# Performance work log

Hardware: AMD Instinct MI355X
Metric: run time of the kernel (lower is better)

Reference implementation:

```python
import jax, jax.numpy as jnp
import numpy as np

N = 100000  # num_nodes


def setup_inputs() -> dict:
    key = jax.random.key(0)
    k1, k2, k3, k4 = jax.random.split(key, 4)
    nodes = jax.random.randint(k1, (10000,), 0, N)
    edge_index = jax.random.randint(k2, (2, 1600000), 0, N)
    emb_weight = jax.random.normal(k3, (N, 512), dtype=jnp.float32)
    W = jax.random.normal(k4, (512, 128), dtype=jnp.float32) * 0.05
    return {"nodes": nodes, "edge_index": edge_index, "emb_weight": emb_weight, "W": W}


def reference(nodes, edge_index, emb_weight, W):
    # GCNConv (PyG semantics, bias=False): add self-loops, symmetric deg
    # normalization, linear transform, scatter-add aggregation into targets.
    num_nodes = emb_weight.shape[0]
    loops = jnp.arange(num_nodes, dtype=edge_index.dtype)
    row = jnp.concatenate([edge_index[0], loops])  # sources (x_j)
    col = jnp.concatenate([edge_index[1], loops])  # targets (aggregation)

    ones = jnp.ones(row.shape[0], dtype=emb_weight.dtype)
    deg = jax.ops.segment_sum(ones, col, num_segments=num_nodes)
    dinv = jnp.where(deg > 0, jax.lax.rsqrt(deg), 0.0)
    norm = dinv[row] * dinv[col]  # [E+N]

    h = emb_weight @ W  # [N, C] dense transform (main GEMM)
    msg = h[row] * norm[:, None]  # gather + scale, [E+N, C]
    out = jax.ops.segment_sum(msg, col, num_segments=num_nodes)  # scatter-add
    return out[nodes]
```

## Files before the change

kernel.cpp:

```cpp
#include <hip/hip_runtime.h>
#include <hip/hip_bf16.h>


constexpr int KDIM = 512;
constexpr int CDIM = 128;
constexpr int CAPB = 64;
constexpr int CAPO = 16;

typedef __attribute__((ext_vector_type(8))) short short8;
typedef __attribute__((ext_vector_type(4))) float f32x4;

static __device__ __forceinline__ unsigned short f2bf(float f) {
    __hip_bfloat16 b = __float2bfloat16(f);
    return *reinterpret_cast<unsigned short*>(&b);
}
static __device__ __forceinline__ float bf2f(unsigned short b) {
    return __uint_as_float(((unsigned)b) << 16);
}

__global__ void k_init(int* __restrict__ deg, int* __restrict__ tmap,
                       int* __restrict__ cur, int* __restrict__ ocnt,
                       int* __restrict__ ucount,
                       const float* __restrict__ W, unsigned short* __restrict__ wt,
                       int N, int n) {
    int i = blockIdx.x * blockDim.x + threadIdx.x;
    if (i < N) { deg[i] = 0; tmap[i] = -1; }
    if (i < n) { cur[i] = 0; ocnt[i] = 0; }
    if (i == 0) *ucount = 0;
    if (i < 65536) {
        int j  = i & 7;
        int l  = (i >> 3) & 63;
        int st = i >> 9;
        int t  = st & 7, s = st >> 3;
        int k  = s * 32 + (l >> 4) * 8 + j;
        int c  = t * 16 + (l & 15);
        wt[i] = f2bf(W[(size_t)k * CDIM + c]);
    }
}

__global__ void k_targets(const int* __restrict__ nodes, int n,
                          int* __restrict__ tmap, int* __restrict__ tlist,
                          int* __restrict__ ucount) {
    int i = blockIdx.x * blockDim.x + threadIdx.x;
    if (i >= n) return;
    int v = nodes[i];
    if (atomicCAS(&tmap[v], -1, -2) == -1) {
        int slot = atomicAdd(ucount, 1);
        tlist[slot] = v;
        tmap[v] = slot;
    }
}

__global__ __launch_bounds__(256, 4)
void k_main(const float* __restrict__ emb, const unsigned short* __restrict__ wt,
            unsigned short* __restrict__ h, int N,
            const int* __restrict__ erow, const int* __restrict__ ecol, int E,
            int* __restrict__ deg, const int* __restrict__ tmap,
            int* __restrict__ cur, int* __restrict__ ebuf,
            const int* __restrict__ nodes, int n,
            int* __restrict__ ocnt, int* __restrict__ olist,
            int GB, int DB) {
    __shared__ float sA[3][64 * 32];
    int bid = (int)blockIdx.x;
    int tid = threadIdx.x;
    if (bid >= GB + DB) {
        int i = (bid - GB - DB) * 256 + tid;
        if (i >= n) return;
        int slot = tmap[nodes[i]];
        int p = atomicAdd(&ocnt[slot], 1);
        if (p < CAPO) olist[slot * CAPO + p] = i;
        return;
    }
    if (bid >= GB) {
        int t = (bid - GB) * 256 + tid;
        int base = t * 4;
        if (base >= E) return;
        if (base + 4 <= E) {
            int4 c = *reinterpret_cast<const int4*>(ecol + base);
            atomicAdd(&deg[c.x], 1);
            atomicAdd(&deg[c.y], 1);
            atomicAdd(&deg[c.z], 1);
            atomicAdd(&deg[c.w], 1);
            int s0 = tmap[c.x], s1 = tmap[c.y], s2 = tmap[c.z], s3 = tmap[c.w];
            if ((s0 >= 0) | (s1 >= 0) | (s2 >= 0) | (s3 >= 0)) {
                int4 r = *reinterpret_cast<const int4*>(erow + base);
                if (s0 >= 0) { int p = atomicAdd(&cur[s0], 1); if (p < CAPB) ebuf[s0 * CAPB + p] = r.x; }
                if (s1 >= 0) { int p = atomicAdd(&cur[s1], 1); if (p < CAPB) ebuf[s1 * CAPB + p] = r.y; }
                if (s2 >= 0) { int p = atomicAdd(&cur[s2], 1); if (p < CAPB) ebuf[s2 * CAPB + p] = r.z; }
                if (s3 >= 0) { int p = atomicAdd(&cur[s3], 1); if (p < CAPB) ebuf[s3 * CAPB + p] = r.w; }
            }
        } else {
            for (int i = base; i < E; ++i) {
                int c = ecol[i];
                atomicAdd(&deg[c], 1);
                int s = tmap[c];
                if (s >= 0) { int p = atomicAdd(&cur[s], 1); if (p < CAPB) ebuf[s * CAPB + p] = erow[i]; }
            }
        }
        return;
    }
    int lane = tid & 63;
    int wid  = tid >> 6;
    int row0 = bid * 64;

    auto stage = [&](int buf, int kc) {
        #pragma unroll
        for (int p = 0; p < 2; ++p) {
            int s = p * 64 + lane;
            int row = s >> 3, chunk = s & 7;
            int swz = chunk ^ (row & 7);
            int rg = row0 + wid * 16 + row; if (rg >= N) rg = N - 1;
            const float* g = emb + (size_t)rg * KDIM + kc * 32 + swz * 4;
            float* l = &sA[buf][(wid * 16 + row) * 32 + chunk * 4];
            __builtin_amdgcn_global_load_lds(
                (const __attribute__((address_space(1))) void*)g,
                (__attribute__((address_space(3))) void*)l, 16, 0, 0);
        }
    };

    f32x4 acc[8];
    #pragma unroll
    for (int t = 0; t < 8; ++t) acc[t] = (f32x4){0.f, 0.f, 0.f, 0.f};

    int arl = lane & 15;
    int al  = wid * 16 + arl;
    int kq  = lane >> 4;

    stage(0, 0); stage(1, 1); stage(2, 2);

    for (int kc = 0; kc < 16; ++kc) {
        if (kc > 0 && kc + 2 < 16) stage((kc + 2) % 3, kc + 2);
        if (kc < 14)       asm volatile("s_waitcnt vmcnt(4)" ::: "memory");
        else if (kc == 14) asm volatile("s_waitcnt vmcnt(2)" ::: "memory");
        else               asm volatile("s_waitcnt vmcnt(0)" ::: "memory");
        const float* Ab = sA[kc % 3];
        int c0 = kq * 2;
        int p0 = c0 ^ (arl & 7);
        int p1 = (c0 + 1) ^ (arl & 7);
        float4 v0 = *reinterpret_cast<const float4*>(Ab + al * 32 + p0 * 4);
        float4 v1 = *reinterpret_cast<const float4*>(Ab + al * 32 + p1 * 4);
        short8 af;
        af[0] = (short)f2bf(v0.x); af[1] = (short)f2bf(v0.y);
        af[2] = (short)f2bf(v0.z); af[3] = (short)f2bf(v0.w);
        af[4] = (short)f2bf(v1.x); af[5] = (short)f2bf(v1.y);
        af[6] = (short)f2bf(v1.z); af[7] = (short)f2bf(v1.w);
        const short8* wp = reinterpret_cast<const short8*>(wt)
                         + (size_t)(kc * 8) * 64 + lane;
        #pragma unroll
        for (int tt = 0; tt < 8; ++tt) {
            short8 bf = wp[tt * 64];
            acc[tt] = __builtin_amdgcn_mfma_f32_16x16x32_bf16(af, bf, acc[tt], 0, 0, 0);
        }
    }

    __syncthreads();
    unsigned short* sC = (unsigned short*)sA;
    int rl0 = wid * 16 + (lane >> 4) * 4;
    int cl0 = lane & 15;
    #pragma unroll
    for (int tt = 0; tt < 8; ++tt)
        #pragma unroll
        for (int j = 0; j < 4; ++j)
            sC[(rl0 + j) * 128 + cl0 + tt * 16] = f2bf(acc[tt][j]);
    __syncthreads();
    #pragma unroll
    for (int c = 0; c < 4; ++c) {
        int i = c * 256 + tid;
        int row = i >> 4, off = i & 15;
        int r = row0 + row;
        if (r < N)
            *reinterpret_cast<short8*>(h + (size_t)r * CDIM + off * 8) =
                *reinterpret_cast<const short8*>(sC + row * 128 + off * 8);
    }
}

__global__ __launch_bounds__(256)
void k_agg(const unsigned short* __restrict__ h, const int* __restrict__ deg,
           const int* __restrict__ tlist, const int* __restrict__ cur,
           const int* __restrict__ ebuf, const int* __restrict__ ucount,
           const int* __restrict__ ocnt, const int* __restrict__ olist,
           float* __restrict__ out) {
    int u = *ucount;
    int slot = blockIdx.x * 4 + (threadIdx.x >> 6);
    if (slot >= u) return;
    int lane = threadIdx.x & 63;
    int e = min(cur[slot], CAPB);
    int myi = 0; float myw = 0.f;
    if (lane < e) {
        myi = ebuf[(size_t)slot * CAPB + lane];
        myw = rsqrtf((float)(deg[myi] + 1));
    }
    int q  = lane >> 4;
    int cl = lane & 15;
    float acc[8];
    #pragma unroll
    for (int x = 0; x < 8; ++x) acc[x] = 0.f;
    int trips = (e + 3) >> 2;
    for (int t = 0; t < trips; ++t) {
        int j = t * 4 + q;
        int   src = __shfl(myi, j, 64);
        float w   = __shfl(myw, j, 64);
        short8 v = *reinterpret_cast<const short8*>(h + (size_t)src * CDIM + cl * 8);
        #pragma unroll
        for (int x = 0; x < 8; ++x)
            acc[x] += w * bf2f((unsigned short)v[x]);
    }
    #pragma unroll
    for (int x = 0; x < 8; ++x) {
        acc[x] += __shfl_xor(acc[x], 16, 64);
        acc[x] += __shfl_xor(acc[x], 32, 64);
    }
    int t = tlist[slot];
    float dt = rsqrtf((float)(deg[t] + 1));
    short8 v = *reinterpret_cast<const short8*>(h + (size_t)t * CDIM + cl * 8);
    float4 r0, r1;
    r0.x = dt * (acc[0] + dt * bf2f((unsigned short)v[0]));
    r0.y = dt * (acc[1] + dt * bf2f((unsigned short)v[1]));
    r0.z = dt * (acc[2] + dt * bf2f((unsigned short)v[2]));
    r0.w = dt * (acc[3] + dt * bf2f((unsigned short)v[3]));
    r1.x = dt * (acc[4] + dt * bf2f((unsigned short)v[4]));
    r1.y = dt * (acc[5] + dt * bf2f((unsigned short)v[5]));
    r1.z = dt * (acc[6] + dt * bf2f((unsigned short)v[6]));
    r1.w = dt * (acc[7] + dt * bf2f((unsigned short)v[7]));
    if (q == 0) {
        int cnt = min(ocnt[slot], CAPO);
        for (int qq = 0; qq < cnt; ++qq) {
            int i = olist[slot * CAPO + qq];
            float* op = out + (size_t)i * CDIM + cl * 8;
            *reinterpret_cast<float4*>(op)     = r0;
            *reinterpret_cast<float4*>(op + 4) = r1;
        }
    }
}

extern "C" void kernel_launch(void* const* d_in, const int* in_sizes, int n_in,
                              void* d_out, int out_size, void* d_ws, size_t ws_size,
                              hipStream_t stream) {
    const int*   nodes = (const int*)d_in[0];
    const int*   eidx  = (const int*)d_in[1];
    const float* emb   = (const float*)d_in[2];
    const float* W     = (const float*)d_in[3];
    float*       out   = (float*)d_out;

    int n = in_sizes[0];
    int E = in_sizes[1] / 2;
    int N = in_sizes[2] / KDIM;
    const int* erow = eidx;
    const int* ecol = eidx + E;

    char* ws = (char*)d_ws;
    size_t o = 0;
    auto carve = [&](size_t bytes) {
        char* p = ws + o;
        o = (o + bytes + 255) & ~(size_t)255;
        return p;
    };
    int* deg    = (int*)carve((size_t)N * 4);
    int* tmap   = (int*)carve((size_t)N * 4);
    int* tlist  = (int*)carve((size_t)n * 4);
    int* cur    = (int*)carve((size_t)n * 4);
    int* ocnt   = (int*)carve((size_t)n * 4);
    int* olist  = (int*)carve((size_t)n * CAPO * 4);
    int* ucount = (int*)carve(4);
    int* ebuf   = (int*)carve((size_t)n * CAPB * 4);
    unsigned short* wt = (unsigned short*)carve((size_t)16 * 8 * 64 * 8 * 2);
    unsigned short* h  = (unsigned short*)carve((size_t)N * CDIM * 2);
    (void)ws_size; (void)n_in; (void)out_size;

    int GB = (N + 63) / 64;
    int DB = (E + 1023) / 1024;
    int OB = (n + 255) / 256;
    k_init   <<<(N + 255) / 256, 256, 0, stream>>>(deg, tmap, cur, ocnt, ucount, W, wt, N, n);
    k_targets<<<(n + 255) / 256, 256, 0, stream>>>(nodes, n, tmap, tlist, ucount);
    k_main   <<<GB + DB + OB, 256, 0, stream>>>(emb, wt, h, N,
                                                erow, ecol, E, deg, tmap, cur, ebuf,
                                                nodes, n, ocnt, olist, GB, DB);
    k_agg    <<<(n + 3) / 4, 256, 0, stream>>>(h, deg, tlist, cur, ebuf, ucount,
                                               ocnt, olist, out);
}
```

Before: 140.8 us.

## Stage full bf16 W in LDS per 1024-thread block, stream A from global into registers

The GEMM kernel now uses 1024-thread blocks, each covering 256 rows. Every block first loads the whole bf16 weight matrix (128 KB) into LDS. The A operand is no longer staged through an LDS triple buffer; it is loaded directly from global memory into registers with a two-step prefetch. B fragments are read from LDS instead of from global or L2 on every step. The trade-offs are that 128 KB of LDS per block allows only one block per CU, the per-block W load up front is exposed, and the A reads have a strided access pattern.

```diff
diff --git a/kernel.cpp b/kernel.cpp
--- a/kernel.cpp
+++ b/kernel.cpp
@@ -51,7 +51,7 @@
     }
 }
 
-__global__ __launch_bounds__(256, 4)
+__global__ __launch_bounds__(1024, 1)
 void k_main(const float* __restrict__ emb, const unsigned short* __restrict__ wt,
             unsigned short* __restrict__ h, int N,
             const int* __restrict__ erow, const int* __restrict__ ecol, int E,
@@ -60,11 +60,10 @@
             const int* __restrict__ nodes, int n,
             int* __restrict__ ocnt, int* __restrict__ olist,
             int GB, int DB) {
-    __shared__ float sA[3][64 * 32];
     int bid = (int)blockIdx.x;
     int tid = threadIdx.x;
     if (bid >= GB + DB) {
-        int i = (bid - GB - DB) * 256 + tid;
+        int i = (bid - GB - DB) * 1024 + tid;
         if (i >= n) return;
         int slot = tmap[nodes[i]];
         int p = atomicAdd(&ocnt[slot], 1);
@@ -72,7 +71,7 @@
         return;
     }
     if (bid >= GB) {
-        int t = (bid - GB) * 256 + tid;
+        int t = (bid - GB) * 1024 + tid;
         int base = t * 4;
         if (base >= E) return;
         if (base + 4 <= E) {
@@ -99,53 +98,55 @@
         }
         return;
     }
+    extern __shared__ char smem[];
+    unsigned short* sBall = (unsigned short*)smem;
     int lane = tid & 63;
     int wid  = tid >> 6;
-    int row0 = bid * 64;
-
-    auto stage = [&](int buf, int kc) {
-        #pragma unroll
-        for (int p = 0; p < 2; ++p) {
-            int s = p * 64 + lane;
-            int row = s >> 3, chunk = s & 7;
-            int swz = chunk ^ (row & 7);
-            int rg = row0 + wid * 16 + row; if (rg >= N) rg = N - 1;
-            const float* g = emb + (size_t)rg * KDIM + kc * 32 + swz * 4;
-            float* l = &sA[buf][(wid * 16 + row) * 32 + chunk * 4];
-            __builtin_amdgcn_global_load_lds(
-                (const __attribute__((address_space(1))) void*)g,
-                (__attribute__((address_space(3))) void*)l, 16, 0, 0);
-        }
-    };
+    int row0 = bid * 256;
+
+    #pragma unroll
+    for (int p = 0; p < 8; ++p) {
+        int i = p * 1024 + tid;
+        const unsigned short* g = wt + (size_t)i * 8;
+        unsigned short* l = sBall + (size_t)i * 8;
+        __builtin_amdgcn_global_load_lds(
+            (const __attribute__((address_space(1))) void*)g,
+            (__attribute__((address_space(3))) void*)l, 16, 0, 0);
+    }
+    asm volatile("s_waitcnt vmcnt(0)" ::: "memory");
+    __builtin_amdgcn_s_barrier();
+
+    int row = row0 + wid * 16 + (lane & 15);
+    if (row >= N) row = N - 1;
+    int kq = lane >> 4;
+    const float* abase = emb + (size_t)row * KDIM + kq * 8;
 
     f32x4 acc[8];
     #pragma unroll
     for (int t = 0; t < 8; ++t) acc[t] = (f32x4){0.f, 0.f, 0.f, 0.f};
 
-    int arl = lane & 15;
-    int al  = wid * 16 + arl;
-    int kq  = lane >> 4;
-
-    stage(0, 0); stage(1, 1); stage(2, 2);
-
-    for (int kc = 0; kc < 16; ++kc) {
-        if (kc > 0 && kc + 2 < 16) stage((kc + 2) % 3, kc + 2);
-        if (kc < 14)       asm volatile("s_waitcnt vmcnt(4)" ::: "memory");
-        else if (kc == 14) asm volatile("s_waitcnt vmcnt(2)" ::: "memory");
-        else               asm volatile("s_waitcnt vmcnt(0)" ::: "memory");
-        const float* Ab = sA[kc % 3];
-        int c0 = kq * 2;
-        int p0 = c0 ^ (arl & 7);
-        int p1 = (c0 + 1) ^ (arl & 7);
-        float4 v0 = *reinterpret_cast<const float4*>(Ab + al * 32 + p0 * 4);
-        float4 v1 = *reinterpret_cast<const float4*>(Ab + al * 32 + p1 * 4);
+    float4 apf0[2], apf1[2];
+    #pragma unroll
+    for (int s = 0; s < 2; ++s) {
+        apf0[s] = *reinterpret_cast<const float4*>(abase + s * 32);
+        apf1[s] = *reinterpret_cast<const float4*>(abase + s * 32 + 4);
+    }
+
+    const short8* Bb = reinterpret_cast<const short8*>(sBall);
+    #pragma unroll
+    for (int ks = 0; ks < 16; ++ks) {
+        float4 v0 = apf0[ks & 1];
+        float4 v1 = apf1[ks & 1];
+        if (ks + 2 < 16) {
+            apf0[ks & 1] = *reinterpret_cast<const float4*>(abase + (ks + 2) * 32);
+            apf1[ks & 1] = *reinterpret_cast<const float4*>(abase + (ks + 2) * 32 + 4);
+        }
         short8 af;
         af[0] = (short)f2bf(v0.x); af[1] = (short)f2bf(v0.y);
         af[2] = (short)f2bf(v0.z); af[3] = (short)f2bf(v0.w);
         af[4] = (short)f2bf(v1.x); af[5] = (short)f2bf(v1.y);
         af[6] = (short)f2bf(v1.z); af[7] = (short)f2bf(v1.w);
-        const short8* wp = reinterpret_cast<const short8*>(wt)
-                         + (size_t)(kc * 8) * 64 + lane;
+        const short8* wp = Bb + (size_t)(ks * 8) * 64 + lane;
         #pragma unroll
         for (int tt = 0; tt < 8; ++tt) {
             short8 bf = wp[tt * 64];
@@ -154,7 +155,7 @@
     }
 
     __syncthreads();
-    unsigned short* sC = (unsigned short*)sA;
+    unsigned short* sC = (unsigned short*)smem;
     int rl0 = wid * 16 + (lane >> 4) * 4;
     int cl0 = lane & 15;
     #pragma unroll
@@ -165,12 +166,12 @@
     __syncthreads();
     #pragma unroll
     for (int c = 0; c < 4; ++c) {
-        int i = c * 256 + tid;
-        int row = i >> 4, off = i & 15;
-        int r = row0 + row;
+        int i = c * 1024 + tid;
+        int r2 = i >> 4, off = i & 15;
+        int r = row0 + r2;
         if (r < N)
             *reinterpret_cast<short8*>(h + (size_t)r * CDIM + off * 8) =
-                *reinterpret_cast<const short8*>(sC + row * 128 + off * 8);
+                *reinterpret_cast<const short8*>(sC + r2 * 128 + off * 8);
     }
 }
 
@@ -267,14 +268,17 @@
     unsigned short* h  = (unsigned short*)carve((size_t)N * CDIM * 2);
     (void)ws_size; (void)n_in; (void)out_size;
 
-    int GB = (N + 63) / 64;
-    int DB = (E + 1023) / 1024;
-    int OB = (n + 255) / 256;
+    hipFuncSetAttribute(reinterpret_cast<const void*>(k_main),
+                        hipFuncAttributeMaxDynamicSharedMemorySize, 131072);
+
+    int GB = (N + 255) / 256;
+    int DB = (E + 4095) / 4096;
+    int OB = (n + 1023) / 1024;
     k_init   <<<(N + 255) / 256, 256, 0, stream>>>(deg, tmap, cur, ocnt, ucount, W, wt, N, n);
     k_targets<<<(n + 255) / 256, 256, 0, stream>>>(nodes, n, tmap, tlist, ucount);
-    k_main   <<<GB + DB + OB, 256, 0, stream>>>(emb, wt, h, N,
-                                                erow, ecol, E, deg, tmap, cur, ebuf,
-                                                nodes, n, ocnt, olist, GB, DB);
+    k_main   <<<GB + DB + OB, 1024, 131072, stream>>>(emb, wt, h, N,
+                                                      erow, ecol, E, deg, tmap, cur, ebuf,
+                                                      nodes, n, ocnt, olist, GB, DB);
     k_agg    <<<(n + 3) / 4, 256, 0, stream>>>(h, deg, tlist, cur, ebuf, ucount,
                                                ocnt, olist, out);
 }
```

After: 134.8 us. 4.3% less time.
